# Performance work log

Measured on AMD Instinct MI355X. Metric: run time of the kernel, lower is better.

The kernel has to match this reference:

```python
import jax, jax.numpy as jnp
import numpy as np

B, S, D, NH, K = 4, 2048, 768, 4, 4
DH = D // NH
EPS = 1e-5


def setup_inputs() -> dict:
    key = jax.random.key(0)
    ks = jax.random.split(key, 10)
    sc = 0.02
    return {
        "x": jax.random.normal(ks[0], (B, S, D), jnp.float32),
        "conv_kernel": jax.random.normal(ks[1], (K, D), jnp.float32) * sc,
        "conv_bias": jnp.zeros((D,), jnp.float32),
        "Wi": jax.random.normal(ks[2], (NH, DH, DH), jnp.float32) * sc,
        "Wf": jax.random.normal(ks[3], (NH, DH, DH), jnp.float32) * sc,
        "Wz": jax.random.normal(ks[4], (NH, DH, DH), jnp.float32) * sc,
        "Wo": jax.random.normal(ks[5], (NH, DH, DH), jnp.float32) * sc,
        "R": jax.random.normal(ks[6], (4, NH, DH, DH), jnp.float32) * sc,
        "cell_bias": jnp.zeros((4, D), jnp.float32),
        "gn_scale": jnp.ones((NH, DH), jnp.float32),
    }


def reference(x, conv_kernel, conv_bias, Wi, Wf, Wz, Wo, R, cell_bias, gn_scale):
    b, s, d = x.shape
    nh, dh, _ = Wi.shape
    k = conv_kernel.shape[0]

    # causal depthwise conv1d + swish
    xc = jax.lax.conv_general_dilated(
        x, conv_kernel[:, None, :], (1,), [(k - 1, 0)],
        dimension_numbers=("NWC", "WIO", "NWC"), feature_group_count=d,
    ) + conv_bias
    x_conv = jax.nn.swish(xc)

    # headwise (block-diagonal) gate projections, no bias
    def headwise(v, W):
        return jnp.einsum("bshd,hde->bshe", v.reshape(b, s, nh, dh), W).reshape(b, s, d)

    i_in = headwise(x_conv, Wi)
    f_in = headwise(x_conv, Wf)
    z_in = headwise(x, Wz)
    o_in = headwise(x, Wo)

    g = jnp.stack([i_in, f_in, z_in, o_in], axis=0).transpose(2, 0, 1, 3)  # (S,4,B,D)

    zeros = jnp.zeros((b, d), x.dtype)
    carry0 = (zeros, zeros, zeros, zeros)  # h, c, n, m

    def step(carry, gt):
        h, c, n, m = carry
        rec = jnp.einsum("bhd,ghde->gbhe", h.reshape(b, nh, dh), R).reshape(4, b, d)
        pre = gt + rec + cell_bias[:, None, :]
        it, ft, zt, ot = pre[0], pre[1], pre[2], pre[3]
        # stabilized exponential gating
        m_new = jnp.maximum(ft + m, it)
        iact = jnp.exp(it - m_new)
        fact = jnp.exp(ft + m - m_new)
        c_new = fact * c + iact * jnp.tanh(zt)
        n_new = fact * n + iact
        h_new = jax.nn.sigmoid(ot) * c_new / n_new
        return (h_new, c_new, n_new, m_new), h_new

    _, ys = jax.lax.scan(step, carry0, g)  # (S,B,D)

    # (B, NH, S, DH) head layout for multi-head layernorm
    y = ys.transpose(1, 0, 2).reshape(b, s, nh, dh).transpose(0, 2, 1, 3)
    mu = y.mean(-1, keepdims=True)
    var = y.var(-1, keepdims=True)
    yn = (y - mu) * jax.lax.rsqrt(var + EPS) * gn_scale[None, :, None, :]
    return yn.transpose(0, 2, 1, 3).reshape(b, s, d)
```

## Files before the change

### kernel.cpp

```cpp
#include <hip/hip_runtime.h>

#define B_  4
#define S_  2048
#define D_  768
#define NH_ 4
#define DH_ 192

typedef short  s8v __attribute__((ext_vector_type(8)));
typedef float  f4v __attribute__((ext_vector_type(4)));
typedef unsigned short ushort_t;

static __device__ __forceinline__ ushort_t f2bf(float f) {
    union { float f; unsigned u; } v; v.f = f;
    unsigned r = v.u + 0x7fffu + ((v.u >> 16) & 1u);
    return (ushort_t)(r >> 16);
}
static __device__ __forceinline__ float bf2f(ushort_t b) {
    union { unsigned u; float f; } v; v.u = ((unsigned)b) << 16;
    return v.f;
}
static __device__ __forceinline__ f4v mfma16(s8v a, s8v b, f4v c) {
    return __builtin_amdgcn_mfma_f32_16x16x32_bf16(a, b, c, 0, 0, 0);
}

__global__ void conv_kernel(const float* __restrict__ x, const float* __restrict__ ck,
                            const float* __restrict__ cb,
                            ushort_t* __restrict__ xconv, ushort_t* __restrict__ xb) {
    int idx = blockIdx.x * blockDim.x + threadIdx.x;
    const int nd4 = D_ / 4;
    int d4 = idx % nd4;
    int bs = idx / nd4;
    int s = bs % S_;
    int b = bs / S_;
    int d = d4 * 4;

    float4 acc = *(const float4*)(cb + d);
    float4 xcur = make_float4(0.f, 0.f, 0.f, 0.f);
#pragma unroll
    for (int k = 0; k < 4; ++k) {
        int sk = s - 3 + k;
        float4 xv = make_float4(0.f, 0.f, 0.f, 0.f);
        if (sk >= 0) xv = *(const float4*)(x + ((size_t)(b * S_ + sk) * D_ + d));
        if (k == 3) xcur = xv;
        float4 kv = *(const float4*)(ck + (size_t)k * D_ + d);
        acc.x += xv.x * kv.x; acc.y += xv.y * kv.y;
        acc.z += xv.z * kv.z; acc.w += xv.w * kv.w;
    }
    float c0 = acc.x / (1.f + __expf(-acc.x));
    float c1 = acc.y / (1.f + __expf(-acc.y));
    float c2 = acc.z / (1.f + __expf(-acc.z));
    float c3 = acc.w / (1.f + __expf(-acc.w));

    size_t base = (size_t)bs * D_ + d;
    ushort4 pc; pc.x = f2bf(c0); pc.y = f2bf(c1); pc.z = f2bf(c2); pc.w = f2bf(c3);
    *(ushort4*)(xconv + base) = pc;
    ushort4 px; px.x = f2bf(xcur.x); px.y = f2bf(xcur.y); px.z = f2bf(xcur.z); px.w = f2bf(xcur.w);
    *(ushort4*)(xb + base) = px;
}

__launch_bounds__(768)
__global__ void gates_kernel(const ushort_t* __restrict__ xconv, const ushort_t* __restrict__ xb,
                             const float* __restrict__ Wi, const float* __restrict__ Wf,
                             const float* __restrict__ Wz, const float* __restrict__ Wo,
                             const float* __restrict__ cbias, ushort_t* __restrict__ G) {
    int sb = blockIdx.x, h = blockIdx.y, p = blockIdx.z;
    const ushort_t* X = (p == 0) ? xconv : xb;
    const float* W0 = (p == 0) ? Wi : Wz;
    const float* W1 = (p == 0) ? Wf : Wo;

    int tid = threadIdx.x;
    int lane = tid & 63;
    int w = tid >> 6;

    int col = w * 16 + (lane & 15);
    int kq0 = (lane >> 4) * 8;

    s8v B0[6], B1[6];
#pragma unroll
    for (int kt = 0; kt < 6; ++kt) {
        const float* w0p = W0 + ((size_t)(h * DH_ + kt * 32 + kq0)) * DH_ + col;
        const float* w1p = W1 + ((size_t)(h * DH_ + kt * 32 + kq0)) * DH_ + col;
        s8v f0, f1;
#pragma unroll
        for (int j = 0; j < 8; ++j) {
            f0[j] = (short)f2bf(w0p[(size_t)j * DH_]);
            f1[j] = (short)f2bf(w1p[(size_t)j * DH_]);
        }
        B0[kt] = f0; B1[kt] = f1;
    }
    float bias0 = cbias[(size_t)(2 * p) * D_ + h * DH_ + col];
    float bias1 = cbias[(size_t)(2 * p + 1) * D_ + h * DH_ + col];

    int b_l = lane & 3;
    int ds_l = (lane >> 2) & 3;

    for (int mt = 0; mt < 16; ++mt) {
        int s = sb * 64 + mt * 4 + ds_l;
        const ushort_t* ap = X + ((size_t)(b_l * S_ + s) * D_ + h * DH_ + kq0);
        s8v A[6];
#pragma unroll
        for (int kt = 0; kt < 6; ++kt) A[kt] = *(const s8v*)(ap + kt * 32);
        f4v a0 = {0.f, 0.f, 0.f, 0.f}, a1 = {0.f, 0.f, 0.f, 0.f};
#pragma unroll
        for (int kt = 0; kt < 6; ++kt) {
            a0 = mfma16(A[kt], B0[kt], a0);
            a1 = mfma16(A[kt], B1[kt], a1);
        }
        int sro = sb * 64 + mt * 4 + (lane >> 4);
#pragma unroll
        for (int r = 0; r < 4; ++r) {
            size_t idx = (((size_t)(sro * NH_ + h) * B_ + r) * DH_ + col) * 4;
            ushort2 pr;
            pr.x = f2bf(a0[r] + bias0);
            pr.y = f2bf(a1[r] + bias1);
            *(ushort2*)(G + idx + 2 * p) = pr;
        }
    }
}

__launch_bounds__(768)
__global__ void recur_kernel(const ushort_t* __restrict__ G, const float* __restrict__ Rw,
                             ushort_t* __restrict__ ys) {
    const int h = blockIdx.x;
    const int tid = threadIdx.x;
    const int lane = tid & 63;
    const int w = tid >> 6;

    __shared__ ushort_t h_lds[2 * 4 * 208];

    s8v Bf[4][6];
    {
        int col = w * 16 + (lane & 15);
        int kq0 = (lane >> 4) * 8;
#pragma unroll
        for (int g = 0; g < 4; ++g)
#pragma unroll
            for (int kt = 0; kt < 6; ++kt) {
                const float* rp = Rw + ((size_t)((g * NH_ + h) * DH_ + kt * 32 + kq0)) * DH_ + col;
                s8v f;
#pragma unroll
                for (int j = 0; j < 8; ++j) f[j] = (short)f2bf(rp[(size_t)j * DH_]);
                Bf[g][kt] = f;
            }
    }

    for (int i = tid; i < 2 * 4 * 208; i += 768) h_lds[i] = 0;

    const int b_id = lane >> 4;
    const int e_id = w * 16 + (lane & 15);
    const int a_off = ((lane & 15) >> 2) * 208 + (lane >> 4) * 8;
    const int hw_off = b_id * 208 + e_id;

    float m_st = 0.f, c_st = 0.f, n_st = 0.f;
    const float LOG2E = 1.44269504088896f;

    const int gstride = NH_ * B_ * DH_ * 4;
    const ushort_t* gp = G + (((size_t)h * B_ + b_id) * DH_ + e_id) * 4;
    ushort4 gv_n = *(const ushort4*)gp;

    ushort_t* yp = ys + ((size_t)h * B_ + b_id) * DH_ + e_id;

    __syncthreads();

    for (int s = 0; s < S_; ++s) {
        ushort4 gv = gv_n;
        if (s + 1 < S_) gp += gstride;
        gv_n = *(const ushort4*)gp;

        const int p = s & 1;
        const ushort_t* abuf = h_lds + p * 832 + a_off;

        s8v A[6];
#pragma unroll
        for (int kt = 0; kt < 6; ++kt)
            A[kt] = *(const s8v*)(abuf + kt * 32);

        f4v acc[4];
#pragma unroll
        for (int g = 0; g < 4; ++g) { acc[g][0] = 0.f; acc[g][1] = 0.f; acc[g][2] = 0.f; acc[g][3] = 0.f; }
#pragma unroll
        for (int kt = 0; kt < 6; ++kt) acc[1] = mfma16(A[kt], Bf[1][kt], acc[1]);
#pragma unroll
        for (int kt = 0; kt < 6; ++kt) acc[0] = mfma16(A[kt], Bf[0][kt], acc[0]);
#pragma unroll
        for (int kt = 0; kt < 6; ++kt) acc[2] = mfma16(A[kt], Bf[2][kt], acc[2]);
#pragma unroll
        for (int kt = 0; kt < 6; ++kt) acc[3] = mfma16(A[kt], Bf[3][kt], acc[3]);

        float it = acc[0][0] + bf2f(gv.x);
        float ft = acc[1][0] + bf2f(gv.y);
        float zt = acc[2][0] + bf2f(gv.z);
        float ot = acc[3][0] + bf2f(gv.w);

        float fm = ft + m_st;
        float mn = fmaxf(fm, it);
        float ia = __builtin_amdgcn_exp2f((it - mn) * LOG2E);
        float fa = __builtin_amdgcn_exp2f((fm - mn) * LOG2E);
        float ez = __builtin_amdgcn_exp2f(zt * (2.f * LOG2E));
        float th = 1.f - 2.f * __builtin_amdgcn_rcpf(ez + 1.f);
        float cn = fa * c_st + ia * th;
        float nn = fa * n_st + ia;
        float sg = __builtin_amdgcn_rcpf(1.f + __builtin_amdgcn_exp2f(-ot * LOG2E));
        float hn = sg * cn * __builtin_amdgcn_rcpf(nn);
        m_st = mn; c_st = cn; n_st = nn;

        ushort_t hb = f2bf(hn);
        h_lds[(1 - p) * 832 + hw_off] = hb;

        asm volatile("s_waitcnt lgkmcnt(0)\n\ts_barrier" ::: "memory");

        *yp = hb;
        yp += NH_ * B_ * DH_;
    }
}

__global__ void ln_kernel(const ushort_t* __restrict__ ys, const float* __restrict__ gn,
                          float* __restrict__ out) {
    int gw = (blockIdx.x * blockDim.x + threadIdx.x) >> 6;
    int lane = threadIdx.x & 63;
    int b = gw & 3;
    int h = (gw >> 2) & 3;
    int s = gw >> 4;

    const ushort_t* yp = ys + (size_t)gw * DH_;
    float v0 = bf2f(yp[lane]);
    float v1 = bf2f(yp[lane + 64]);
    float v2 = bf2f(yp[lane + 128]);
    float sum = v0 + v1 + v2;
    float sq  = v0 * v0 + v1 * v1 + v2 * v2;
#pragma unroll
    for (int off = 32; off > 0; off >>= 1) {
        sum += __shfl_xor(sum, off, 64);
        sq  += __shfl_xor(sq,  off, 64);
    }
    float mu  = sum * (1.f / 192.f);
    float var = sq * (1.f / 192.f) - mu * mu;
    float rs  = rsqrtf(var + 1e-5f);

    float* op = out + (size_t)(b * S_ + s) * D_ + h * DH_;
    const float* gp = gn + h * DH_;
    op[lane]       = (v0 - mu) * rs * gp[lane];
    op[lane + 64]  = (v1 - mu) * rs * gp[lane + 64];
    op[lane + 128] = (v2 - mu) * rs * gp[lane + 128];
}

extern "C" void kernel_launch(void* const* d_in, const int* in_sizes, int n_in,
                              void* d_out, int out_size, void* d_ws, size_t ws_size,
                              hipStream_t stream) {
    const float* x     = (const float*)d_in[0];
    const float* ck    = (const float*)d_in[1];
    const float* cb    = (const float*)d_in[2];
    const float* Wi    = (const float*)d_in[3];
    const float* Wf    = (const float*)d_in[4];
    const float* Wz    = (const float*)d_in[5];
    const float* Wo    = (const float*)d_in[6];
    const float* Rw    = (const float*)d_in[7];
    const float* cbias = (const float*)d_in[8];
    const float* gn    = (const float*)d_in[9];
    float* out = (float*)d_out;

    const size_t nBSD = (size_t)B_ * S_ * D_;
    ushort_t* xconv = (ushort_t*)d_ws;
    ushort_t* xb    = xconv + nBSD;
    ushort_t* G     = xb + nBSD;
    ushort_t* ys    = G + (size_t)S_ * NH_ * 4 * B_ * DH_;

    conv_kernel<<<dim3(B_ * S_ * D_ / 4 / 256), dim3(256), 0, stream>>>(x, ck, cb, xconv, xb);
    gates_kernel<<<dim3(32, NH_, 2), dim3(768), 0, stream>>>(xconv, xb, Wi, Wf, Wz, Wo, cbias, G);
    recur_kernel<<<dim3(NH_), dim3(768), 0, stream>>>(G, Rw, ys);
    ln_kernel<<<dim3(8192), dim3(256), 0, stream>>>(ys, gn, out);
}
```

Before: 2.042 ms.

## Split each head's recurrence across two workgroups with global-memory flag exchange

The recurrence for each head is split across two workgroups, each owning half of the 192 output columns. Within a workgroup, the K reduction is split between two wave groups. One group reads the local half of h from LDS. The other spins on tagged atomic loads from a global ring buffer written by the partner workgroup. The goal is to halve per-CU MFMA work and register pressure on the serial critical path, at the cost of a cross-CU handshake every timestep. The launch also rounds up to 16 blocks, where the mapping from block index to CU decides whether partners run concurrently. Workspace buffers are reused, and a zero kernel clears the flag buffer.

```diff
diff --git a/kernel.cpp b/kernel.cpp
--- a/kernel.cpp
+++ b/kernel.cpp
@@ -118,99 +118,147 @@
     }
 }
 
+__global__ void zero_kernel(unsigned* __restrict__ z) {
+    for (int i = threadIdx.x; i < 3072; i += 256) z[i] = 0;
+}
+
 __launch_bounds__(768)
 __global__ void recur_kernel(const ushort_t* __restrict__ G, const float* __restrict__ Rw,
-                             ushort_t* __restrict__ ys) {
-    const int h = blockIdx.x;
+                             ushort_t* __restrict__ ys, unsigned* __restrict__ xbuf) {
+    const int bid = blockIdx.x;
+    const int head = bid & 7;
+    if (head >= NH_) return;
+    const int half = bid >> 3;
+
     const int tid = threadIdx.x;
     const int lane = tid & 63;
-    const int w = tid >> 6;
-
-    __shared__ ushort_t h_lds[2 * 4 * 208];
-
-    s8v Bf[4][6];
-    {
-        int col = w * 16 + (lane & 15);
-        int kq0 = (lane >> 4) * 8;
-#pragma unroll
-        for (int g = 0; g < 4; ++g)
-#pragma unroll
-            for (int kt = 0; kt < 6; ++kt) {
-                const float* rp = Rw + ((size_t)((g * NH_ + h) * DH_ + kt * 32 + kq0)) * DH_ + col;
-                s8v f;
-#pragma unroll
-                for (int j = 0; j < 8; ++j) f[j] = (short)f2bf(rp[(size_t)j * DH_]);
-                Bf[g][kt] = f;
-            }
-    }
-
-    for (int i = tid; i < 2 * 4 * 208; i += 768) h_lds[i] = 0;
-
-    const int b_id = lane >> 4;
-    const int e_id = w * 16 + (lane & 15);
-    const int a_off = ((lane & 15) >> 2) * 208 + (lane >> 4) * 8;
-    const int hw_off = b_id * 208 + e_id;
+    const int wv = tid >> 6;
+    const int et = wv >> 1;
+    const int kh = wv & 1;
+    const int c = lane & 15;
+    const int t = lane >> 4;
+
+    __shared__ ushort_t h_lds[2][4][104];
+    __shared__ f4v psum[6][64];
+
+    const int e_col = half * 96 + et * 16 + c;
+    const int k_src = (kh == 0) ? half * 96 : (1 - half) * 96;
+
+    s8v Bf[4][3];
+#pragma unroll
+    for (int g = 0; g < 4; ++g)
+#pragma unroll
+        for (int ktl = 0; ktl < 3; ++ktl) {
+            const float* rp = Rw + ((size_t)((g * NH_ + head) * DH_ + k_src + ktl * 32 + t * 8)) * DH_ + e_col;
+            s8v f;
+#pragma unroll
+            for (int j = 0; j < 8; ++j) f[j] = (short)f2bf(rp[(size_t)j * DH_]);
+            Bf[g][ktl] = f;
+        }
+
+    for (int i = tid; i < 2 * 4 * 104; i += 768) (&h_lds[0][0][0])[i] = 0;
+
+    const int b_id = t;
+    const int e_loc = et * 16 + c;
 
     float m_st = 0.f, c_st = 0.f, n_st = 0.f;
     const float LOG2E = 1.44269504088896f;
 
+    unsigned* const xw = xbuf + (size_t)head * 768 + (size_t)half * 384 + b_id * 96 + e_loc;
+    const unsigned* const xr = xbuf + (size_t)head * 768 + (size_t)(1 - half) * 384
+                                    + (c >> 2) * 96 + t * 8;
+
     const int gstride = NH_ * B_ * DH_ * 4;
-    const ushort_t* gp = G + (((size_t)h * B_ + b_id) * DH_ + e_id) * 4;
-    ushort4 gv_n = *(const ushort4*)gp;
-
-    ushort_t* yp = ys + ((size_t)h * B_ + b_id) * DH_ + e_id;
+    const ushort_t* gp = G + (((size_t)head * B_ + b_id) * DH_ + e_col) * 4;
+    ushort4 gv_n = make_ushort4(0, 0, 0, 0);
+    if (kh == 0) gv_n = *(const ushort4*)gp;
+
+    ushort_t* yp = ys + ((size_t)head * B_ + b_id) * DH_ + e_col;
 
     __syncthreads();
 
     for (int s = 0; s < S_; ++s) {
-        ushort4 gv = gv_n;
-        if (s + 1 < S_) gp += gstride;
-        gv_n = *(const ushort4*)gp;
-
         const int p = s & 1;
-        const ushort_t* abuf = h_lds + p * 832 + a_off;
-
-        s8v A[6];
-#pragma unroll
-        for (int kt = 0; kt < 6; ++kt)
-            A[kt] = *(const s8v*)(abuf + kt * 32);
+        ushort4 gv = make_ushort4(0, 0, 0, 0);
+        s8v A[3];
+
+        if (kh == 0) {
+            gv = gv_n;
+            if (s + 1 < S_) gp += gstride;
+            gv_n = *(const ushort4*)gp;
+            const ushort_t* ab = &h_lds[p][c >> 2][t * 8];
+#pragma unroll
+            for (int ktl = 0; ktl < 3; ++ktl)
+                A[ktl] = *(const s8v*)(ab + ktl * 32);
+        } else {
+            const unsigned* rb = xr + (size_t)(s & 7) * 3072;
+            unsigned dw[3][8];
+            for (;;) {
+                bool ok = true;
+#pragma unroll
+                for (int ktl = 0; ktl < 3; ++ktl)
+#pragma unroll
+                    for (int j = 0; j < 8; ++j) {
+                        dw[ktl][j] = __hip_atomic_load(rb + ktl * 32 + j,
+                                         __ATOMIC_RELAXED, __HIP_MEMORY_SCOPE_SYSTEM);
+                        ok = ok && ((int)(dw[ktl][j] >> 16) == s);
+                    }
+                if (ok) break;
+            }
+#pragma unroll
+            for (int ktl = 0; ktl < 3; ++ktl) {
+                s8v a;
+#pragma unroll
+                for (int j = 0; j < 8; ++j) a[j] = (short)(dw[ktl][j] & 0xffffu);
+                A[ktl] = a;
+            }
+        }
 
         f4v acc[4];
 #pragma unroll
         for (int g = 0; g < 4; ++g) { acc[g][0] = 0.f; acc[g][1] = 0.f; acc[g][2] = 0.f; acc[g][3] = 0.f; }
 #pragma unroll
-        for (int kt = 0; kt < 6; ++kt) acc[1] = mfma16(A[kt], Bf[1][kt], acc[1]);
-#pragma unroll
-        for (int kt = 0; kt < 6; ++kt) acc[0] = mfma16(A[kt], Bf[0][kt], acc[0]);
-#pragma unroll
-        for (int kt = 0; kt < 6; ++kt) acc[2] = mfma16(A[kt], Bf[2][kt], acc[2]);
-#pragma unroll
-        for (int kt = 0; kt < 6; ++kt) acc[3] = mfma16(A[kt], Bf[3][kt], acc[3]);
-
-        float it = acc[0][0] + bf2f(gv.x);
-        float ft = acc[1][0] + bf2f(gv.y);
-        float zt = acc[2][0] + bf2f(gv.z);
-        float ot = acc[3][0] + bf2f(gv.w);
-
-        float fm = ft + m_st;
-        float mn = fmaxf(fm, it);
-        float ia = __builtin_amdgcn_exp2f((it - mn) * LOG2E);
-        float fa = __builtin_amdgcn_exp2f((fm - mn) * LOG2E);
-        float ez = __builtin_amdgcn_exp2f(zt * (2.f * LOG2E));
-        float th = 1.f - 2.f * __builtin_amdgcn_rcpf(ez + 1.f);
-        float cn = fa * c_st + ia * th;
-        float nn = fa * n_st + ia;
-        float sg = __builtin_amdgcn_rcpf(1.f + __builtin_amdgcn_exp2f(-ot * LOG2E));
-        float hn = sg * cn * __builtin_amdgcn_rcpf(nn);
-        m_st = mn; c_st = cn; n_st = nn;
-
-        ushort_t hb = f2bf(hn);
-        h_lds[(1 - p) * 832 + hw_off] = hb;
-
+        for (int ktl = 0; ktl < 3; ++ktl)
+#pragma unroll
+            for (int g = 0; g < 4; ++g)
+                acc[g] = mfma16(A[ktl], Bf[g][ktl], acc[g]);
+
+        if (kh == 1) {
+            f4v v; v[0] = acc[0][0]; v[1] = acc[1][0]; v[2] = acc[2][0]; v[3] = acc[3][0];
+            psum[et][lane] = v;
+        }
         asm volatile("s_waitcnt lgkmcnt(0)\n\ts_barrier" ::: "memory");
 
-        *yp = hb;
-        yp += NH_ * B_ * DH_;
+        if (kh == 0) {
+            f4v rd = psum[et][lane];
+            float it = acc[0][0] + rd[0] + bf2f(gv.x);
+            float ft = acc[1][0] + rd[1] + bf2f(gv.y);
+            float zt = acc[2][0] + rd[2] + bf2f(gv.z);
+            float ot = acc[3][0] + rd[3] + bf2f(gv.w);
+
+            float fm = ft + m_st;
+            float mn = fmaxf(fm, it);
+            float ia = __builtin_amdgcn_exp2f((it - mn) * LOG2E);
+            float fa = __builtin_amdgcn_exp2f((fm - mn) * LOG2E);
+            float ez = __builtin_amdgcn_exp2f(zt * (2.f * LOG2E));
+            float th = 1.f - 2.f * __builtin_amdgcn_rcpf(ez + 1.f);
+            float cn = fa * c_st + ia * th;
+            float nn = fa * n_st + ia;
+            float sg = __builtin_amdgcn_rcpf(1.f + __builtin_amdgcn_exp2f(-ot * LOG2E));
+            float hn = sg * cn * __builtin_amdgcn_rcpf(nn);
+            m_st = mn; c_st = cn; n_st = nn;
+
+            ushort_t hb = f2bf(hn);
+            h_lds[1 - p][b_id][e_loc] = hb;
+
+            __hip_atomic_store(xw + (size_t)((s + 1) & 7) * 3072,
+                               ((unsigned)(s + 1) << 16) | (unsigned)hb,
+                               __ATOMIC_RELAXED, __HIP_MEMORY_SCOPE_SYSTEM);
+            *yp = hb;
+            yp += NH_ * B_ * DH_;
+        }
+
+        asm volatile("s_waitcnt lgkmcnt(0)\n\ts_barrier" ::: "memory");
     }
 }
 
@@ -263,10 +311,12 @@
     ushort_t* xconv = (ushort_t*)d_ws;
     ushort_t* xb    = xconv + nBSD;
     ushort_t* G     = xb + nBSD;
-    ushort_t* ys    = G + (size_t)S_ * NH_ * 4 * B_ * DH_;
+    ushort_t* ys    = xconv;
+    unsigned* xbuf  = (unsigned*)xb;
 
     conv_kernel<<<dim3(B_ * S_ * D_ / 4 / 256), dim3(256), 0, stream>>>(x, ck, cb, xconv, xb);
     gates_kernel<<<dim3(32, NH_, 2), dim3(768), 0, stream>>>(xconv, xb, Wi, Wf, Wz, Wo, cbias, G);
-    recur_kernel<<<dim3(NH_), dim3(768), 0, stream>>>(G, Rw, ys);
+    zero_kernel<<<dim3(1), dim3(256), 0, stream>>>(xbuf);
+    recur_kernel<<<dim3(16), dim3(768), 0, stream>>>(G, Rw, ys, xbuf);
     ln_kernel<<<dim3(8192), dim3(256), 0, stream>>>(ys, gn, out);
 }
```

After: 4.223 ms. 107% more time.
